# Kernel tuning notes

Hardware: AMD Instinct MI355X
Metric: run time of the kernel (lower is better)

Reference implementation:

```python
import jax, jax.numpy as jnp
import numpy as np

# Module config (from init_kwargs)
B, S = 2, 2048            # batch, prompt length
NH, D = 16, 64            # num query heads, head_size
NKV = 4                   # num kv heads
QPK = NH // NKV           # queries per kv head (GQA)
BLOCK = 128               # paged KV-cache block size
NBLOCKS = 64              # total cache blocks
SCALE = 0.125             # 1/sqrt(D)
NEG = -1e9                # causal mask value (finite for grad safety)


def setup_inputs() -> dict:
    key = jax.random.key(0)
    k1, k2, k3 = jax.random.split(key, 3)
    query = jax.random.normal(k1, (B, S, NH * D), jnp.float32)
    key_t = jax.random.normal(k2, (B, S, NKV * D), jnp.float32)
    value = jax.random.normal(k3, (B, S, NKV * D), jnp.float32)
    # kv_cache = [2, num_blocks, block_size, num_kv_heads, head_size]
    kv_cache = jnp.zeros((2, NBLOCKS, BLOCK, NKV, D), jnp.float32)
    # causal attn_bias [B, 1, 1, S, S] as set by the vLLM model runner
    i = jnp.arange(S)
    causal = jnp.where(i[None, :] <= i[:, None], 0.0, NEG).astype(jnp.float32)
    attn_bias = jnp.broadcast_to(causal[None, None, None], (B, 1, 1, S, S))
    # standard alibi slopes for 16 heads: 2^(-0.5*(h+1))
    alibi_slopes = 2.0 ** (-0.5 * (jnp.arange(NH, dtype=jnp.float32) + 1.0))
    # prompt writes B*S/BLOCK = 32 full blocks into the cache
    block_indices = jnp.arange(B * S // BLOCK, dtype=jnp.int32)
    return {"query": query, "key": key_t, "value": value, "kv_cache": kv_cache,
            "attn_bias": attn_bias, "alibi_slopes": alibi_slopes,
            "block_indices": block_indices}


def reference(query, key, value, kv_cache, attn_bias, alibi_slopes, block_indices):
    Bq, Sq, _ = query.shape
    q = query.reshape(Bq, Sq, NKV, QPK, D)   # [b, i, h, g, d]
    k = key.reshape(Bq, Sq, NKV, D)          # [b, j, h, d]
    v = value.reshape(Bq, Sq, NKV, D)

    # --- paged KV-cache scatter (VLLMKVCache.insert_or_update_cache, prompt path) ---
    k_blocks = key.reshape(-1, BLOCK, NKV, D)   # [n_used_blocks, block, h, d]
    v_blocks = value.reshape(-1, BLOCK, NKV, D)
    key_cache = kv_cache[0].at[block_indices].set(k_blocks)
    value_cache = kv_cache[1].at[block_indices].set(v_blocks)

    # --- _make_alibi_bias: (j - i) * slope, unflattened to [1, Hkv, qpk, S, S] ---
    ar = jnp.arange(Sq)
    diff = (ar[None, :] - ar[:, None]).astype(query.dtype)        # [S, S]
    pos_bias = alibi_slopes[:, None, None] * diff                  # [NH, S, S]
    pos_bias = pos_bias.reshape(1, NKV, QPK, Sq, Sq)
    bias = attn_bias + pos_bias                                    # [B, Hkv, qpk, S, S]

    # --- prompt_attention: matmul_qk -> softmax -> matmul_av (GQA) ---
    scores = jnp.einsum('bihgd,bjhd->bhgij', q, k) * SCALE + bias
    attn = jax.nn.softmax(scores, axis=-1)
    out = jnp.einsum('bhgij,bjhd->bihgd', attn, v).reshape(Bq, Sq, NH * D)
    return out, key_cache, value_cache
```

## Files before the change

kernel.cpp:

```cpp
#include <hip/hip_runtime.h>
#include <hip/hip_bf16.h>
#include <math.h>

#define BB    2
#define SS    2048
#define NHh   16
#define DD    64
#define NKV   4
#define BLKV  128
#define SCALE 0.125f

#define KT    64

typedef __attribute__((ext_vector_type(8))) short short8;
typedef __attribute__((ext_vector_type(4))) float f32x4;
typedef __attribute__((ext_vector_type(4))) int   i32x4;

template<int N> struct IC { static constexpr int v = N; };

__device__ inline short bf16c(float x) {
  __hip_bfloat16 h = __float2bfloat16(x);
  return *reinterpret_cast<short*>(&h);
}

__device__ inline int pk_bf16(float a, float b) {
  int d;
  asm("v_cvt_pk_bf16_f32 %0, %1, %2" : "=v"(d) : "v"(a), "v"(b));
  return d;
}

#define GLL16(g, l) __builtin_amdgcn_global_load_lds( \
    (const __attribute__((address_space(1))) void*)(g), \
    (__attribute__((address_space(3))) void*)(l), 16, 0, 0)

__global__ __launch_bounds__(256) void aux_kernel(
    const float* __restrict__ k, const float* __restrict__ v,
    const float* __restrict__ kvc, const int* __restrict__ bidx, int nidx,
    unsigned short* __restrict__ kimg, unsigned short* __restrict__ vimg,
    float* __restrict__ kc, float* __restrict__ vc)
{
  const int wg  = blockIdx.x;
  const int tid = threadIdx.x;
  if (wg < BB * NKV * (SS / KT)) {
    const int t   = wg & 31;
    const int hkv = (wg >> 5) & 3;
    const int b   = wg >> 7;
    const int j0  = t * KT;
    const float* kp = k + ((size_t)(b * SS + j0) * NKV + hkv) * DD;
    const float* vp = v + ((size_t)(b * SS + j0) * NKV + hkv) * DD;
    unsigned short* ki = kimg + (size_t)wg * 4096;
    unsigned short* vi = vimg + (size_t)wg * 4096;
    const int bi    = bidx[b * 16 + (t >> 1)];
    const int rowc0 = (t & 1) * 64;
    float* kcb = kc + (size_t)bi * (BLKV * NKV * DD);
    float* vcb = vc + (size_t)bi * (BLKV * NKV * DD);

    {
      const int jj = tid >> 2;
      const int sb = (tid & 3) * 2;
#pragma unroll
      for (int ss = 0; ss < 2; ++ss) {
        const int s  = sb + ss;
        const int d0 = (s ^ (jj & 7)) * 8;
        const float4 a = *(const float4*)(kp + jj * (NKV * DD) + d0);
        const float4 c = *(const float4*)(kp + jj * (NKV * DD) + d0 + 4);
        *(short8*)&ki[jj * 64 + s * 8] =
            (short8){bf16c(a.x), bf16c(a.y), bf16c(a.z), bf16c(a.w),
                     bf16c(c.x), bf16c(c.y), bf16c(c.z), bf16c(c.w)};
        float* kd = kcb + (rowc0 + jj) * (NKV * DD) + hkv * DD + d0;
        *(float4*)kd       = a;
        *(float4*)(kd + 4) = c;
      }
    }
    {
      const int d = tid & 63;
      const int w = tid >> 6;
#pragma unroll
      for (int ji = 0; ji < 2; ++ji) {
        const int jb = w * 2 + ji;
        float vv[8];
#pragma unroll
        for (int e = 0; e < 8; ++e)
          vv[e] = vp[(jb * 8 + e) * (NKV * DD) + d];
        const int s = jb ^ (d & 7);
        *(short8*)&vi[d * 64 + s * 8] =
            (short8){bf16c(vv[0]), bf16c(vv[1]), bf16c(vv[2]), bf16c(vv[3]),
                     bf16c(vv[4]), bf16c(vv[5]), bf16c(vv[6]), bf16c(vv[7])};
#pragma unroll
        for (int e = 0; e < 8; ++e)
          vcb[(rowc0 + jb * 8 + e) * (NKV * DD) + hkv * DD + d] = vv[e];
      }
    }
  } else {
    const int w2    = wg - BB * NKV * (SS / KT);
    const int blk   = w2 & 63;
    const int plane = w2 >> 6;
    int covered = 0;
    for (int m = 0; m < nidx; ++m) covered |= (bidx[m] == blk);
    if (covered) return;
    const float4* s4 = (const float4*)(kvc + (size_t)plane * (64 * BLKV * NKV * DD)
                                           + (size_t)blk * (BLKV * NKV * DD));
    float4* d4 = (float4*)((plane ? vc : kc) + (size_t)blk * (BLKV * NKV * DD));
#pragma unroll 4
    for (int i = tid; i < (BLKV * NKV * DD) / 4; i += 256) d4[i] = s4[i];
  }
}

__global__ __launch_bounds__(256) void attn_kernel(
    const float* __restrict__ q, const unsigned short* __restrict__ kimg,
    const unsigned short* __restrict__ vimg, const float* __restrict__ slopes,
    float* __restrict__ out)
{
  __shared__ __align__(16) unsigned short Kbuf[2][4096];
  __shared__ __align__(16) unsigned short Vbuf[2][4096];

  const int tid  = threadIdx.x;
  const int wave = tid >> 6;
  const int lane = tid & 63;
  const int cl   = lane & 15;
  const int g    = lane >> 4;

  const int grp   = blockIdx.x & 7;
  const int b     = grp >> 2;
  const int hkv   = grp & 3;
  const int local = blockIdx.x >> 3;
  const int h     = hkv * 4 + (local & 3);
  const int qt    = 31 - (local >> 2);

  const float L2E    = 1.44269504088896340736f;
  const float slope2 = slopes[h] * L2E;
  const float SC2    = SCALE * L2E;
  const int q_blk = qt * 64;
  const int q0    = q_blk + wave * 16;
  const int iq    = q0 + cl;

  short8 qf[2];
  {
    const float* qp = q + ((size_t)(b * SS + iq) * NHh + h) * DD;
#pragma unroll
    for (int kq = 0; kq < 2; ++kq) {
      const int d0 = kq * 32 + g * 8;
      const float4 a = *(const float4*)(qp + d0);
      const float4 c = *(const float4*)(qp + d0 + 4);
      qf[kq] = (short8){bf16c(a.x), bf16c(a.y), bf16c(a.z), bf16c(a.w),
                        bf16c(c.x), bf16c(c.y), bf16c(c.z), bf16c(c.w)};
    }
  }

  const float slope16 = slope2 * 16.f;
  const float slope64 = slope2 * 64.f;
  float ab = -slope2 * (float)iq;
  float cst[4];
#pragma unroll
  for (int r = 0; r < 4; ++r) cst[r] = slope2 * (float)(4 * g + r);

  const int src0 = cl + ((g & 1) << 5);
  const int src1 = src0 + 16;
  const bool gEven = (g < 2);

  float m_ = -INFINITY, l_ = 0.f;
  f32x4 acc[4];
#pragma unroll
  for (int dt = 0; dt < 4; ++dt) acc[dt] = (f32x4){0.f, 0.f, 0.f, 0.f};

  const char* kt0 = (const char*)kimg + (size_t)((b * NKV + hkv) * 32) * 8192;
  const char* vt0 = (const char*)vimg + (size_t)((b * NKV + hkv) * 32) * 8192;
  const int goff0 = wave * 2048 + lane * 16;
  const int ldst0 = wave * 2048;

  auto stage = [&](auto BUFC, int t) {
    constexpr int B = decltype(BUFC)::v;
    const char* kt = kt0 + (size_t)t * 8192 + goff0;
    const char* vt = vt0 + (size_t)t * 8192 + goff0;
    GLL16(kt,        (char*)&Kbuf[B][0] + ldst0);
    GLL16(kt + 1024, (char*)&Kbuf[B][0] + ldst0 + 1024);
    GLL16(vt,        (char*)&Vbuf[B][0] + ldst0);
    GLL16(vt + 1024, (char*)&Vbuf[B][0] + ldst0 + 1024);
  };

  auto tile = [&](auto BUFC, auto MSKC, int t) {
    constexpr int B    = decltype(BUFC)::v;
    constexpr bool MSK = decltype(MSKC)::v;
    const unsigned short* Kb = Kbuf[B];
    const unsigned short* Vb = Vbuf[B];

    f32x4 sc[4];
    __builtin_amdgcn_s_setprio(1);
#pragma unroll
    for (int jt = 0; jt < 4; ++jt) {
      const int rb = (jt * 16 + cl) * 64;
      const short8 kfA = *(const short8*)&Kb[rb + ((g       ^ (cl & 7)) << 3)];
      const short8 kfB = *(const short8*)&Kb[rb + (((4 | g) ^ (cl & 7)) << 3)];
      f32x4 s = (f32x4){0.f, 0.f, 0.f, 0.f};
      s = __builtin_amdgcn_mfma_f32_16x16x32_bf16(kfA, qf[0], s, 0, 0, 0);
      s = __builtin_amdgcn_mfma_f32_16x16x32_bf16(kfB, qf[1], s, 0, 0, 0);
      sc[jt] = s;
    }
    __builtin_amdgcn_s_setprio(0);

    float pm = -INFINITY;
#pragma unroll
    for (int jt = 0; jt < 4; ++jt) {
      const float ajt = ab + slope16 * (float)jt;
#pragma unroll
      for (int r = 0; r < 4; ++r) {
        float val = fmaf(sc[jt][r], SC2, ajt + cst[r]);
        if (MSK) {
          const int j = t * 64 + jt * 16 + 4 * g + r;
          val = (j <= iq) ? val : -INFINITY;
        }
        sc[jt][r] = val;
        pm = fmaxf(pm, val);
      }
    }
    pm = fmaxf(pm, __shfl_xor(pm, 16));
    pm = fmaxf(pm, __shfl_xor(pm, 32));

    if (!__all(pm - m_ <= 11.5f)) {
      const float mn = fmaxf(m_, pm);
      const float sf = exp2f(m_ - mn);
      m_ = mn;
      l_ *= sf;
#pragma unroll
      for (int dt = 0; dt < 4; ++dt)
#pragma unroll
        for (int r = 0; r < 4; ++r) acc[dt][r] *= sf;
    }

    float rs = 0.f;
#pragma unroll
    for (int jt = 0; jt < 4; ++jt) {
#pragma unroll
      for (int r = 0; r < 4; ++r) {
        const float p = exp2f(sc[jt][r] - m_);
        sc[jt][r] = p;
        rs += p;
      }
    }
    rs += __shfl_xor(rs, 16);
    rs += __shfl_xor(rs, 32);
    l_ += rs;

    __builtin_amdgcn_s_setprio(1);
#pragma unroll
    for (int ks = 0; ks < 2; ++ks) {
      const int E0 = pk_bf16(sc[2 * ks][0],     sc[2 * ks][1]);
      const int E1 = pk_bf16(sc[2 * ks][2],     sc[2 * ks][3]);
      const int O0 = pk_bf16(sc[2 * ks + 1][0], sc[2 * ks + 1][1]);
      const int O1 = pk_bf16(sc[2 * ks + 1][2], sc[2 * ks + 1][3]);
      const int d0e = __shfl(E0, src0), d0o = __shfl(O0, src0);
      const int d1e = __shfl(E1, src0), d1o = __shfl(O1, src0);
      const int d2e = __shfl(E0, src1), d2o = __shfl(O0, src1);
      const int d3e = __shfl(E1, src1), d3o = __shfl(O1, src1);
      i32x4 pd;
      pd[0] = gEven ? d0e : d0o;
      pd[1] = gEven ? d1e : d1o;
      pd[2] = gEven ? d2e : d2o;
      pd[3] = gEven ? d3e : d3o;
      const short8 pb = *(const short8*)&pd;
#pragma unroll
      for (int dt = 0; dt < 4; ++dt) {
        const short8 va = *(const short8*)
            &Vb[(dt * 16 + cl) * 64 + ((((ks << 2) | g) ^ (cl & 7)) << 3)];
        acc[dt] = __builtin_amdgcn_mfma_f32_16x16x32_bf16(va, pb, acc[dt], 0, 0, 0);
      }
    }
    __builtin_amdgcn_s_setprio(0);

    ab += slope64;
  };

  stage(IC<0>{}, 0);
  __syncthreads();

  const int nt = qt + 1;
  const int NU = nt - 1;
  int t = 0;
  while (t + 2 <= NU) {
    stage(IC<1>{}, t + 1);
    tile(IC<0>{}, IC<0>{}, t);
    __syncthreads();
    stage(IC<0>{}, t + 2);
    tile(IC<1>{}, IC<0>{}, t + 1);
    __syncthreads();
    t += 2;
  }
  if (t < NU) {
    stage(IC<1>{}, t + 1);
    tile(IC<0>{}, IC<0>{}, t);
    __syncthreads();
    tile(IC<1>{}, IC<1>{}, t + 1);
  } else {
    tile(IC<0>{}, IC<1>{}, t);
  }

  const float inv = 1.f / l_;
  float* op = out + ((size_t)(b * SS + iq) * NHh + h) * DD + 4 * g;
#pragma unroll
  for (int dt = 0; dt < 4; ++dt) {
    float4 o4;
    o4.x = acc[dt][0] * inv;
    o4.y = acc[dt][1] * inv;
    o4.z = acc[dt][2] * inv;
    o4.w = acc[dt][3] * inv;
    *(float4*)(op + dt * 16) = o4;
  }
}

extern "C" void kernel_launch(void* const* d_in, const int* in_sizes, int n_in,
                              void* d_out, int out_size, void* d_ws, size_t ws_size,
                              hipStream_t stream) {
  const float* q      = (const float*)d_in[0];
  const float* k      = (const float*)d_in[1];
  const float* v      = (const float*)d_in[2];
  const float* kvc    = (const float*)d_in[3];
  const float* slopes = (const float*)d_in[5];
  const int*   bidx   = (const int*)d_in[6];

  float* out = (float*)d_out;
  float* kc  = out + BB * SS * NHh * DD;
  float* vc  = kc + 64 * BLKV * NKV * DD;

  unsigned short* kimg = (unsigned short*)d_ws;
  unsigned short* vimg = kimg + (size_t)BB * NKV * 32 * 4096;

  const int nidx = in_sizes[6];

  aux_kernel<<<dim3(256 + 128), dim3(256), 0, stream>>>(
      k, v, kvc, bidx, nidx, kimg, vimg, kc, vc);

  attn_kernel<<<dim3(1024), dim3(256), 0, stream>>>(q, kimg, vimg, slopes, out);
}
```

Before: 65.62 us.

## Software-pipeline QK and PV across tiles with triple-buffered LDS

Restructures the attention main loop so the QK matmul of tile t is issued alongside the PV matmul of tile t-1, with the softmax of tile t following. The accumulator rescale is deferred until just before the next PV. LDS goes from double to triple buffering so the prefetch of tile t+1 can proceed during this overlap. The aim is to hide softmax/exp latency behind MFMA work. In exchange it uses more LDS and registers, and buffers are now chosen through runtime pointers instead of compile-time template constants, which may reduce occupancy or hurt code generation.

New measurement: 70.72 us. +7.8%, slower.

```diff
diff --git a/kernel.cpp b/kernel.cpp
--- a/kernel.cpp
+++ b/kernel.cpp
@@ -15,8 +15,6 @@
 typedef __attribute__((ext_vector_type(8))) short short8;
 typedef __attribute__((ext_vector_type(4))) float f32x4;
 typedef __attribute__((ext_vector_type(4))) int   i32x4;
-
-template<int N> struct IC { static constexpr int v = N; };
 
 __device__ inline short bf16c(float x) {
   __hip_bfloat16 h = __float2bfloat16(x);
@@ -111,8 +109,8 @@
     const unsigned short* __restrict__ vimg, const float* __restrict__ slopes,
     float* __restrict__ out)
 {
-  __shared__ __align__(16) unsigned short Kbuf[2][4096];
-  __shared__ __align__(16) unsigned short Vbuf[2][4096];
+  __shared__ __align__(16) unsigned short KB[3][4096];
+  __shared__ __align__(16) unsigned short VB[3][4096];
 
   const int tid  = threadIdx.x;
   const int wave = tid >> 6;
@@ -159,32 +157,29 @@
   const bool gEven = (g < 2);
 
   float m_ = -INFINITY, l_ = 0.f;
+  float sfp = 1.f;
+  bool  pend = false;
   f32x4 acc[4];
 #pragma unroll
   for (int dt = 0; dt < 4; ++dt) acc[dt] = (f32x4){0.f, 0.f, 0.f, 0.f};
+  short8 pb0, pb1;
+  f32x4 sc[4];
 
   const char* kt0 = (const char*)kimg + (size_t)((b * NKV + hkv) * 32) * 8192;
   const char* vt0 = (const char*)vimg + (size_t)((b * NKV + hkv) * 32) * 8192;
   const int goff0 = wave * 2048 + lane * 16;
   const int ldst0 = wave * 2048;
 
-  auto stage = [&](auto BUFC, int t) {
-    constexpr int B = decltype(BUFC)::v;
+  auto stage = [&](unsigned short* kb, unsigned short* vb, int t) {
     const char* kt = kt0 + (size_t)t * 8192 + goff0;
     const char* vt = vt0 + (size_t)t * 8192 + goff0;
-    GLL16(kt,        (char*)&Kbuf[B][0] + ldst0);
-    GLL16(kt + 1024, (char*)&Kbuf[B][0] + ldst0 + 1024);
-    GLL16(vt,        (char*)&Vbuf[B][0] + ldst0);
-    GLL16(vt + 1024, (char*)&Vbuf[B][0] + ldst0 + 1024);
-  };
-
-  auto tile = [&](auto BUFC, auto MSKC, int t) {
-    constexpr int B    = decltype(BUFC)::v;
-    constexpr bool MSK = decltype(MSKC)::v;
-    const unsigned short* Kb = Kbuf[B];
-    const unsigned short* Vb = Vbuf[B];
-
-    f32x4 sc[4];
+    GLL16(kt,        (char*)kb + ldst0);
+    GLL16(kt + 1024, (char*)kb + ldst0 + 1024);
+    GLL16(vt,        (char*)vb + ldst0);
+    GLL16(vt + 1024, (char*)vb + ldst0 + 1024);
+  };
+
+  auto qk = [&](const unsigned short* Kb) {
     __builtin_amdgcn_s_setprio(1);
 #pragma unroll
     for (int jt = 0; jt < 4; ++jt) {
@@ -197,34 +192,59 @@
       sc[jt] = s;
     }
     __builtin_amdgcn_s_setprio(0);
-
-    float pm = -INFINITY;
+  };
+
+  auto rescale = [&]() {
+    if (pend) {
+#pragma unroll
+      for (int dt = 0; dt < 4; ++dt)
+#pragma unroll
+        for (int r = 0; r < 4; ++r) acc[dt][r] *= sfp;
+      pend = false;
+    }
+  };
+
+  auto pv = [&](const unsigned short* Vb) {
+    __builtin_amdgcn_s_setprio(1);
+#pragma unroll
+    for (int ks = 0; ks < 2; ++ks) {
+      const short8 pbk = ks ? pb1 : pb0;
+#pragma unroll
+      for (int dt = 0; dt < 4; ++dt) {
+        const short8 va = *(const short8*)
+            &Vb[(dt * 16 + cl) * 64 + ((((ks << 2) | g) ^ (cl & 7)) << 3)];
+        acc[dt] = __builtin_amdgcn_mfma_f32_16x16x32_bf16(va, pbk, acc[dt], 0, 0, 0);
+      }
+    }
+    __builtin_amdgcn_s_setprio(0);
+  };
+
+  auto softmax = [&](int t, bool msk) {
+    float mj[4];
 #pragma unroll
     for (int jt = 0; jt < 4; ++jt) {
       const float ajt = ab + slope16 * (float)jt;
 #pragma unroll
       for (int r = 0; r < 4; ++r) {
         float val = fmaf(sc[jt][r], SC2, ajt + cst[r]);
-        if (MSK) {
+        if (msk) {
           const int j = t * 64 + jt * 16 + 4 * g + r;
           val = (j <= iq) ? val : -INFINITY;
         }
         sc[jt][r] = val;
-        pm = fmaxf(pm, val);
-      }
-    }
+      }
+      mj[jt] = fmaxf(fmaxf(sc[jt][0], sc[jt][1]), fmaxf(sc[jt][2], sc[jt][3]));
+    }
+    float pm = fmaxf(fmaxf(mj[0], mj[1]), fmaxf(mj[2], mj[3]));
     pm = fmaxf(pm, __shfl_xor(pm, 16));
     pm = fmaxf(pm, __shfl_xor(pm, 32));
 
     if (!__all(pm - m_ <= 11.5f)) {
       const float mn = fmaxf(m_, pm);
-      const float sf = exp2f(m_ - mn);
+      sfp = exp2f(m_ - mn);
       m_ = mn;
-      l_ *= sf;
-#pragma unroll
-      for (int dt = 0; dt < 4; ++dt)
-#pragma unroll
-        for (int r = 0; r < 4; ++r) acc[dt][r] *= sf;
+      l_ *= sfp;
+      pend = true;
     }
 
     float rs = 0.f;
@@ -241,7 +261,6 @@
     rs += __shfl_xor(rs, 32);
     l_ += rs;
 
-    __builtin_amdgcn_s_setprio(1);
 #pragma unroll
     for (int ks = 0; ks < 2; ++ks) {
       const int E0 = pk_bf16(sc[2 * ks][0],     sc[2 * ks][1]);
@@ -257,42 +276,36 @@
       pd[1] = gEven ? d1e : d1o;
       pd[2] = gEven ? d2e : d2o;
       pd[3] = gEven ? d3e : d3o;
-      const short8 pb = *(const short8*)&pd;
-#pragma unroll
-      for (int dt = 0; dt < 4; ++dt) {
-        const short8 va = *(const short8*)
-            &Vb[(dt * 16 + cl) * 64 + ((((ks << 2) | g) ^ (cl & 7)) << 3)];
-        acc[dt] = __builtin_amdgcn_mfma_f32_16x16x32_bf16(va, pb, acc[dt], 0, 0, 0);
-      }
-    }
-    __builtin_amdgcn_s_setprio(0);
-
+      if (ks == 0) pb0 = *(const short8*)&pd;
+      else         pb1 = *(const short8*)&pd;
+    }
     ab += slope64;
   };
 
-  stage(IC<0>{}, 0);
+  const int NU = qt;
+  stage(&KB[0][0], &VB[0][0], 0);
+  if (NU >= 1) stage(&KB[1][0], &VB[1][0], 1);
   __syncthreads();
 
-  const int nt = qt + 1;
-  const int NU = nt - 1;
-  int t = 0;
-  while (t + 2 <= NU) {
-    stage(IC<1>{}, t + 1);
-    tile(IC<0>{}, IC<0>{}, t);
+  qk(&KB[0][0]);
+  softmax(0, NU == 0);
+
+  unsigned short *kcur = &KB[1][0], *kprv = &KB[0][0], *knxt = &KB[2][0];
+  unsigned short *vcur = &VB[1][0], *vprv = &VB[0][0], *vnxt = &VB[2][0];
+
+  for (int t = 1; t <= NU; ++t) {
+    qk(kcur);
+    if (t < NU) stage(knxt, vnxt, t + 1);
+    rescale();
+    pv(vprv);
+    softmax(t, t == NU);
     __syncthreads();
-    stage(IC<0>{}, t + 2);
-    tile(IC<1>{}, IC<0>{}, t + 1);
-    __syncthreads();
-    t += 2;
+    unsigned short* tk = kprv; kprv = kcur; kcur = knxt; knxt = tk;
+    unsigned short* tv = vprv; vprv = vcur; vcur = vnxt; vnxt = tv;
   }
-  if (t < NU) {
-    stage(IC<1>{}, t + 1);
-    tile(IC<0>{}, IC<0>{}, t);
-    __syncthreads();
-    tile(IC<1>{}, IC<1>{}, t + 1);
-  } else {
-    tile(IC<0>{}, IC<1>{}, t);
-  }
+
+  rescale();
+  pv(vprv);
 
   const float inv = 1.f / l_;
   float* op = out + ((size_t)(b * SS + iq) * NHh + h) * DD + 4 * g;
```

## Pair short and long causal query tiles per workgroup with split-KV merge

Applied to the files above, without the earlier changes.

Each 512-thread workgroup now handles two query tiles, a short one (p) and a long one (31-p), so causal work is balanced across workgroups. Both wave groups share the K/V stream up to the short tile. After that, the second tile's KV range is split by column halves between the two groups, and the partial softmax results are merged through shared memory. This removes the tail imbalance of the triangular workload. The cost is larger workgroups, an extra LDS merge phase and half-width MFMA work per group in the second phase.

After: 64.10 us. 2.3% less time.

```diff
diff --git a/kernel.cpp b/kernel.cpp
--- a/kernel.cpp
+++ b/kernel.cpp
@@ -106,36 +106,41 @@
   }
 }
 
-__global__ __launch_bounds__(256) void attn_kernel(
+__global__ __launch_bounds__(512) void attn_kernel(
     const float* __restrict__ q, const unsigned short* __restrict__ kimg,
     const unsigned short* __restrict__ vimg, const float* __restrict__ slopes,
     float* __restrict__ out)
 {
-  __shared__ __align__(16) unsigned short Kbuf[2][4096];
-  __shared__ __align__(16) unsigned short Vbuf[2][4096];
+  __shared__ __align__(16) char smem[2 * 16384];
 
   const int tid  = threadIdx.x;
   const int wave = tid >> 6;
   const int lane = tid & 63;
   const int cl   = lane & 15;
   const int g    = lane >> 4;
+  const int group = wave >> 2;
+  const int wi    = wave & 3;
 
   const int grp   = blockIdx.x & 7;
   const int b     = grp >> 2;
   const int hkv   = grp & 3;
   const int local = blockIdx.x >> 3;
   const int h     = hkv * 4 + (local & 3);
-  const int qt    = 31 - (local >> 2);
+  const int p     = local >> 2;
+  const int qtA   = p;
+  const int qtB   = 31 - p;
 
   const float L2E    = 1.44269504088896340736f;
   const float slope2 = slopes[h] * L2E;
   const float SC2    = SCALE * L2E;
-  const int q_blk = qt * 64;
-  const int q0    = q_blk + wave * 16;
-  const int iq    = q0 + cl;
+  const float slope16 = slope2 * 16.f;
+  const float slope64 = slope2 * 64.f;
+
+  int myqt = group ? qtB : qtA;
+  int iq   = myqt * 64 + wi * 16 + cl;
 
   short8 qf[2];
-  {
+  auto loadQ = [&]() {
     const float* qp = q + ((size_t)(b * SS + iq) * NHh + h) * DD;
 #pragma unroll
     for (int kq = 0; kq < 2; ++kq) {
@@ -145,10 +150,9 @@
       qf[kq] = (short8){bf16c(a.x), bf16c(a.y), bf16c(a.z), bf16c(a.w),
                         bf16c(c.x), bf16c(c.y), bf16c(c.z), bf16c(c.w)};
     }
-  }
-
-  const float slope16 = slope2 * 16.f;
-  const float slope64 = slope2 * 64.f;
+  };
+  loadQ();
+
   float ab = -slope2 * (float)iq;
   float cst[4];
 #pragma unroll
@@ -165,29 +169,25 @@
 
   const char* kt0 = (const char*)kimg + (size_t)((b * NKV + hkv) * 32) * 8192;
   const char* vt0 = (const char*)vimg + (size_t)((b * NKV + hkv) * 32) * 8192;
-  const int goff0 = wave * 2048 + lane * 16;
-  const int ldst0 = wave * 2048;
-
-  auto stage = [&](auto BUFC, int t) {
-    constexpr int B = decltype(BUFC)::v;
-    const char* kt = kt0 + (size_t)t * 8192 + goff0;
-    const char* vt = vt0 + (size_t)t * 8192 + goff0;
-    GLL16(kt,        (char*)&Kbuf[B][0] + ldst0);
-    GLL16(kt + 1024, (char*)&Kbuf[B][0] + ldst0 + 1024);
-    GLL16(vt,        (char*)&Vbuf[B][0] + ldst0);
-    GLL16(vt + 1024, (char*)&Vbuf[B][0] + ldst0 + 1024);
+
+  auto stage = [&](int buf, int t) {
+    char* base = smem + buf * 16384 + wave * 1024;
+    const char* src = kt0 + (size_t)t * 8192 + wave * 1024 + lane * 16;
+    const char* srv = vt0 + (size_t)t * 8192 + wave * 1024 + lane * 16;
+    GLL16(src, base);
+    GLL16(srv, base + 8192);
   };
 
-  auto tile = [&](auto BUFC, auto MSKC, int t) {
-    constexpr int B    = decltype(BUFC)::v;
-    constexpr bool MSK = decltype(MSKC)::v;
-    const unsigned short* Kb = Kbuf[B];
-    const unsigned short* Vb = Vbuf[B];
+  auto tcore = [&](auto JTBC, auto JTEC, int buf, int t, bool msk) {
+    constexpr int JTB = decltype(JTBC)::v;
+    constexpr int JTE = decltype(JTEC)::v;
+    const unsigned short* Kb = (const unsigned short*)(smem + buf * 16384);
+    const unsigned short* Vb = (const unsigned short*)(smem + buf * 16384 + 8192);
 
     f32x4 sc[4];
     __builtin_amdgcn_s_setprio(1);
 #pragma unroll
-    for (int jt = 0; jt < 4; ++jt) {
+    for (int jt = JTB; jt < JTE; ++jt) {
       const int rb = (jt * 16 + cl) * 64;
       const short8 kfA = *(const short8*)&Kb[rb + ((g       ^ (cl & 7)) << 3)];
       const short8 kfB = *(const short8*)&Kb[rb + (((4 | g) ^ (cl & 7)) << 3)];
@@ -198,20 +198,29 @@
     }
     __builtin_amdgcn_s_setprio(0);
 
+#pragma unroll
+    for (int jt = JTB; jt < JTE; ++jt) {
+      const float ajt = ab + slope16 * (float)jt;
+#pragma unroll
+      for (int r = 0; r < 4; ++r)
+        sc[jt][r] = fmaf(sc[jt][r], SC2, ajt + cst[r]);
+    }
+    if (msk) {
+#pragma unroll
+      for (int jt = JTB; jt < JTE; ++jt)
+#pragma unroll
+        for (int r = 0; r < 4; ++r) {
+          const int j = t * 64 + jt * 16 + 4 * g + r;
+          if (j > iq) sc[jt][r] = -INFINITY;
+        }
+    }
+
     float pm = -INFINITY;
 #pragma unroll
-    for (int jt = 0; jt < 4; ++jt) {
-      const float ajt = ab + slope16 * (float)jt;
-#pragma unroll
-      for (int r = 0; r < 4; ++r) {
-        float val = fmaf(sc[jt][r], SC2, ajt + cst[r]);
-        if (MSK) {
-          const int j = t * 64 + jt * 16 + 4 * g + r;
-          val = (j <= iq) ? val : -INFINITY;
-        }
-        sc[jt][r] = val;
-        pm = fmaxf(pm, val);
-      }
+    for (int jt = JTB; jt < JTE; ++jt) {
+      const float a01 = fmaxf(sc[jt][0], sc[jt][1]);
+      const float a23 = fmaxf(sc[jt][2], sc[jt][3]);
+      pm = fmaxf(pm, fmaxf(a01, a23));
     }
     pm = fmaxf(pm, __shfl_xor(pm, 16));
     pm = fmaxf(pm, __shfl_xor(pm, 32));
@@ -229,21 +238,20 @@
 
     float rs = 0.f;
 #pragma unroll
-    for (int jt = 0; jt < 4; ++jt) {
+    for (int jt = JTB; jt < JTE; ++jt)
 #pragma unroll
       for (int r = 0; r < 4; ++r) {
-        const float p = exp2f(sc[jt][r] - m_);
-        sc[jt][r] = p;
-        rs += p;
+        const float pp = exp2f(sc[jt][r] - m_);
+        sc[jt][r] = pp;
+        rs += pp;
       }
-    }
     rs += __shfl_xor(rs, 16);
     rs += __shfl_xor(rs, 32);
     l_ += rs;
 
     __builtin_amdgcn_s_setprio(1);
 #pragma unroll
-    for (int ks = 0; ks < 2; ++ks) {
+    for (int ks = JTB / 2; ks < JTE / 2; ++ks) {
       const int E0 = pk_bf16(sc[2 * ks][0],     sc[2 * ks][1]);
       const int E1 = pk_bf16(sc[2 * ks][2],     sc[2 * ks][3]);
       const int O0 = pk_bf16(sc[2 * ks + 1][0], sc[2 * ks + 1][1]);
@@ -270,40 +278,80 @@
     ab += slope64;
   };
 
-  stage(IC<0>{}, 0);
+  int buf = 0;
+  stage(0, 0);
   __syncthreads();
-
-  const int nt = qt + 1;
-  const int NU = nt - 1;
-  int t = 0;
-  while (t + 2 <= NU) {
-    stage(IC<1>{}, t + 1);
-    tile(IC<0>{}, IC<0>{}, t);
+  for (int t = 0; t <= qtA; ++t) {
+    stage(buf ^ 1, t + 1);
+    tcore(IC<0>{}, IC<4>{}, buf, t, (group == 0) && (t == qtA));
     __syncthreads();
-    stage(IC<0>{}, t + 2);
-    tile(IC<1>{}, IC<0>{}, t + 1);
+    buf ^= 1;
+  }
+
+  if (group == 0) {
+    const float inv = 1.f / l_;
+    float* op = out + ((size_t)(b * SS + iq) * NHh + h) * DD + 4 * g;
+#pragma unroll
+    for (int dt = 0; dt < 4; ++dt) {
+      float4 o4;
+      o4.x = acc[dt][0] * inv;
+      o4.y = acc[dt][1] * inv;
+      o4.z = acc[dt][2] * inv;
+      o4.w = acc[dt][3] * inv;
+      *(float4*)(op + dt * 16) = o4;
+    }
+    iq = qtB * 64 + wi * 16 + cl;
+    loadQ();
+    m_ = -INFINITY; l_ = 0.f;
+#pragma unroll
+    for (int dt = 0; dt < 4; ++dt) acc[dt] = (f32x4){0.f, 0.f, 0.f, 0.f};
+    ab = slope2 * (float)(64 * (qtA + 1) - iq);
+  }
+
+  for (int t = qtA + 1; t <= qtB; ++t) {
+    if (t < qtB) stage(buf ^ 1, t + 1);
+    const bool msk = (t == qtB);
+    if (group) tcore(IC<2>{}, IC<4>{}, buf, t, msk);
+    else       tcore(IC<0>{}, IC<2>{}, buf, t, msk);
     __syncthreads();
-    t += 2;
-  }
-  if (t < NU) {
-    stage(IC<1>{}, t + 1);
-    tile(IC<0>{}, IC<0>{}, t);
-    __syncthreads();
-    tile(IC<1>{}, IC<1>{}, t + 1);
-  } else {
-    tile(IC<0>{}, IC<1>{}, t);
-  }
-
-  const float inv = 1.f / l_;
-  float* op = out + ((size_t)(b * SS + iq) * NHh + h) * DD + 4 * g;
-#pragma unroll
-  for (int dt = 0; dt < 4; ++dt) {
-    float4 o4;
-    o4.x = acc[dt][0] * inv;
-    o4.y = acc[dt][1] * inv;
-    o4.z = acc[dt][2] * inv;
-    o4.w = acc[dt][3] * inv;
-    *(float4*)(op + dt * 16) = o4;
+    buf ^= 1;
+  }
+
+  float* accA = (float*)smem;
+  float* mlA  = (float*)(smem + 4 * 16 * 72 * 4);
+  if (group == 0) {
+    float* ar = accA + (wi * 16 + cl) * 72 + 4 * g;
+#pragma unroll
+    for (int dt = 0; dt < 4; ++dt) {
+      float4 a4;
+      a4.x = acc[dt][0]; a4.y = acc[dt][1]; a4.z = acc[dt][2]; a4.w = acc[dt][3];
+      *(float4*)(ar + dt * 16) = a4;
+    }
+    if (g == 0) {
+      mlA[(wi * 2 + 0) * 16 + cl] = m_;
+      mlA[(wi * 2 + 1) * 16 + cl] = l_;
+    }
+  }
+  __syncthreads();
+  if (group == 1) {
+    const float mA = mlA[(wi * 2 + 0) * 16 + cl];
+    const float lA = mlA[(wi * 2 + 1) * 16 + cl];
+    const float M  = fmaxf(m_, mA);
+    const float eB = exp2f(m_ - M);
+    const float eA = exp2f(mA - M);
+    const float inv = 1.f / (l_ * eB + lA * eA);
+    const float* ar = accA + (wi * 16 + cl) * 72 + 4 * g;
+    float* op = out + ((size_t)(b * SS + iq) * NHh + h) * DD + 4 * g;
+#pragma unroll
+    for (int dt = 0; dt < 4; ++dt) {
+      const float4 a4 = *(const float4*)(ar + dt * 16);
+      float4 o4;
+      o4.x = (acc[dt][0] * eB + a4.x * eA) * inv;
+      o4.y = (acc[dt][1] * eB + a4.y * eA) * inv;
+      o4.z = (acc[dt][2] * eB + a4.z * eA) * inv;
+      o4.w = (acc[dt][3] * eB + a4.w * eA) * inv;
+      *(float4*)(op + dt * 16) = o4;
+    }
   }
 }
 
@@ -329,5 +377,5 @@
   aux_kernel<<<dim3(256 + 128), dim3(256), 0, stream>>>(
       k, v, kvc, bidx, nidx, kimg, vimg, kc, vc);
 
-  attn_kernel<<<dim3(1024), dim3(256), 0, stream>>>(q, kimg, vimg, slopes, out);
-}
+  attn_kernel<<<dim3(512), dim3(512), 0, stream>>>(q, kimg, vimg, slopes, out);
+}
```

## Switch attention to 32x32x16 MFMA with split-KV waves and merged softmax

Applied to the files above, without the earlier changes.

Replaces the 16x16x32 MFMA tiling with 32x32x16 MFMAs. Each pair of waves now shares 32 query rows and splits each 64-key tile into two 32-key halves, and the two partial softmax states are merged through LDS at the end. The aux kernel writes K and V into a single interleaved, MFMA-fragment-ordered image per tile, so LDS reads become plain lane-contiguous loads with no swizzle. The aim is fewer MFMA issues and cross-lane shuffles, at the cost of an extra LDS reduction and barrier, and one wave idling on the diagonal tile.

New measurement: 72.43 us. 1.1x slower.

```diff
diff --git a/kernel.cpp b/kernel.cpp
--- a/kernel.cpp
+++ b/kernel.cpp
@@ -10,11 +10,9 @@
 #define BLKV  128
 #define SCALE 0.125f
 
-#define KT    64
-
-typedef __attribute__((ext_vector_type(8))) short short8;
-typedef __attribute__((ext_vector_type(4))) float f32x4;
-typedef __attribute__((ext_vector_type(4))) int   i32x4;
+typedef __attribute__((ext_vector_type(8)))  short short8;
+typedef __attribute__((ext_vector_type(16))) float f32x16;
+typedef __attribute__((ext_vector_type(4)))  int   i32x4;
 
 template<int N> struct IC { static constexpr int v = N; };
 
@@ -36,45 +34,44 @@
 __global__ __launch_bounds__(256) void aux_kernel(
     const float* __restrict__ k, const float* __restrict__ v,
     const float* __restrict__ kvc, const int* __restrict__ bidx, int nidx,
-    unsigned short* __restrict__ kimg, unsigned short* __restrict__ vimg,
-    float* __restrict__ kc, float* __restrict__ vc)
+    char* __restrict__ img, float* __restrict__ kc, float* __restrict__ vc)
 {
   const int wg  = blockIdx.x;
   const int tid = threadIdx.x;
-  if (wg < BB * NKV * (SS / KT)) {
+  if (wg < BB * NKV * 32) {
     const int t   = wg & 31;
     const int hkv = (wg >> 5) & 3;
     const int b   = wg >> 7;
-    const int j0  = t * KT;
-    const float* kp = k + ((size_t)(b * SS + j0) * NKV + hkv) * DD;
-    const float* vp = v + ((size_t)(b * SS + j0) * NKV + hkv) * DD;
-    unsigned short* ki = kimg + (size_t)wg * 4096;
-    unsigned short* vi = vimg + (size_t)wg * 4096;
+    const float* kp = k + ((size_t)(b * SS + t * 64) * NKV + hkv) * DD;
+    const float* vp = v + ((size_t)(b * SS + t * 64) * NKV + hkv) * DD;
+    char* ti = img + (size_t)wg * 16384;
     const int bi    = bidx[b * 16 + (t >> 1)];
     const int rowc0 = (t & 1) * 64;
     float* kcb = kc + (size_t)bi * (BLKV * NKV * DD);
     float* vcb = vc + (size_t)bi * (BLKV * NKV * DD);
 
     {
-      const int jj = tid >> 2;
-      const int sb = (tid & 3) * 2;
-#pragma unroll
-      for (int ss = 0; ss < 2; ++ss) {
-        const int s  = sb + ss;
-        const int d0 = (s ^ (jj & 7)) * 8;
-        const float4 a = *(const float4*)(kp + jj * (NKV * DD) + d0);
-        const float4 c = *(const float4*)(kp + jj * (NKV * DD) + d0 + 4);
-        *(short8*)&ki[jj * 64 + s * 8] =
+      const int jg  = tid & 63;
+      const int cs2 = tid >> 6;
+#pragma unroll
+      for (int ch = 0; ch < 2; ++ch) {
+        const int c  = cs2 * 2 + ch;
+        const int d0 = c * 8;
+        const float4 a  = *(const float4*)(kp + jg * (NKV * DD) + d0);
+        const float4 cc = *(const float4*)(kp + jg * (NKV * DD) + d0 + 4);
+        *(short8*)(ti + (jg >> 5) * 4096 + (cs2 * 64 + ch * 32 + (jg & 31)) * 16) =
             (short8){bf16c(a.x), bf16c(a.y), bf16c(a.z), bf16c(a.w),
-                     bf16c(c.x), bf16c(c.y), bf16c(c.z), bf16c(c.w)};
-        float* kd = kcb + (rowc0 + jj) * (NKV * DD) + hkv * DD + d0;
+                     bf16c(cc.x), bf16c(cc.y), bf16c(cc.z), bf16c(cc.w)};
+        float* kd = kcb + (rowc0 + jg) * (NKV * DD) + hkv * DD + d0;
         *(float4*)kd       = a;
-        *(float4*)(kd + 4) = c;
+        *(float4*)(kd + 4) = cc;
       }
     }
     {
-      const int d = tid & 63;
-      const int w = tid >> 6;
+      const int d   = tid & 63;
+      const int w   = tid >> 6;
+      const int dt  = d >> 5;
+      const int d32 = d & 31;
 #pragma unroll
       for (int ji = 0; ji < 2; ++ji) {
         const int jb = w * 2 + ji;
@@ -82,8 +79,9 @@
 #pragma unroll
         for (int e = 0; e < 8; ++e)
           vv[e] = vp[(jb * 8 + e) * (NKV * DD) + d];
-        const int s = jb ^ (d & 7);
-        *(short8*)&vi[d * 64 + s * 8] =
+        const int half = jb >> 2, qq = jb & 3, ks = qq >> 1, h2 = qq & 1;
+        *(short8*)(ti + 8192 + half * 4096 +
+                   ((dt * 2 + ks) * 64 + h2 * 32 + d32) * 16) =
             (short8){bf16c(vv[0]), bf16c(vv[1]), bf16c(vv[2]), bf16c(vv[3]),
                      bf16c(vv[4]), bf16c(vv[5]), bf16c(vv[6]), bf16c(vv[7])};
 #pragma unroll
@@ -92,7 +90,7 @@
       }
     }
   } else {
-    const int w2    = wg - BB * NKV * (SS / KT);
+    const int w2    = wg - BB * NKV * 32;
     const int blk   = w2 & 63;
     const int plane = w2 >> 6;
     int covered = 0;
@@ -107,113 +105,101 @@
 }
 
 __global__ __launch_bounds__(256) void attn_kernel(
-    const float* __restrict__ q, const unsigned short* __restrict__ kimg,
-    const unsigned short* __restrict__ vimg, const float* __restrict__ slopes,
-    float* __restrict__ out)
+    const float* __restrict__ q, const char* __restrict__ img,
+    const float* __restrict__ slopes, float* __restrict__ out)
 {
-  __shared__ __align__(16) unsigned short Kbuf[2][4096];
-  __shared__ __align__(16) unsigned short Vbuf[2][4096];
+  __shared__ __align__(16) char smem[2 * 16384];
 
   const int tid  = threadIdx.x;
   const int wave = tid >> 6;
   const int lane = tid & 63;
-  const int cl   = lane & 15;
-  const int g    = lane >> 4;
+  const int ql   = lane & 31;
+  const int h2   = lane >> 5;
+  const int half = wave & 1;
+  const int qsel = wave >> 1;
 
   const int grp   = blockIdx.x & 7;
   const int b     = grp >> 2;
   const int hkv   = grp & 3;
   const int local = blockIdx.x >> 3;
-  const int h     = hkv * 4 + (local & 3);
+  const int hh    = hkv * 4 + (local & 3);
   const int qt    = 31 - (local >> 2);
 
   const float L2E    = 1.44269504088896340736f;
-  const float slope2 = slopes[h] * L2E;
+  const float slope2 = slopes[hh] * L2E;
   const float SC2    = SCALE * L2E;
-  const int q_blk = qt * 64;
-  const int q0    = q_blk + wave * 16;
-  const int iq    = q0 + cl;
-
-  short8 qf[2];
+  const int qbase = qt * 64 + qsel * 32;
+  const int qrow  = qbase + ql;
+
+  short8 qf[4];
   {
-    const float* qp = q + ((size_t)(b * SS + iq) * NHh + h) * DD;
-#pragma unroll
-    for (int kq = 0; kq < 2; ++kq) {
-      const int d0 = kq * 32 + g * 8;
+    const float* qp = q + ((size_t)(b * SS + qrow) * NHh + hh) * DD;
+#pragma unroll
+    for (int ks = 0; ks < 4; ++ks) {
+      const int d0 = ks * 16 + h2 * 8;
       const float4 a = *(const float4*)(qp + d0);
       const float4 c = *(const float4*)(qp + d0 + 4);
-      qf[kq] = (short8){bf16c(a.x), bf16c(a.y), bf16c(a.z), bf16c(a.w),
+      qf[ks] = (short8){bf16c(a.x), bf16c(a.y), bf16c(a.z), bf16c(a.w),
                         bf16c(c.x), bf16c(c.y), bf16c(c.z), bf16c(c.w)};
     }
   }
 
-  const float slope16 = slope2 * 16.f;
-  const float slope64 = slope2 * 64.f;
-  float ab = -slope2 * (float)iq;
-  float cst[4];
-#pragma unroll
-  for (int r = 0; r < 4; ++r) cst[r] = slope2 * (float)(4 * g + r);
-
-  const int src0 = cl + ((g & 1) << 5);
-  const int src1 = src0 + 16;
-  const bool gEven = (g < 2);
+  const int jqoff = half * 32 + 4 * h2 - qrow;
+  float sl_lo[4], sl_hi[4];
+#pragma unroll
+  for (int i = 0; i < 4; ++i) { sl_lo[i] = slope2 * i; sl_hi[i] = slope2 * (8 * i); }
 
   float m_ = -INFINITY, l_ = 0.f;
-  f32x4 acc[4];
-#pragma unroll
-  for (int dt = 0; dt < 4; ++dt) acc[dt] = (f32x4){0.f, 0.f, 0.f, 0.f};
-
-  const char* kt0 = (const char*)kimg + (size_t)((b * NKV + hkv) * 32) * 8192;
-  const char* vt0 = (const char*)vimg + (size_t)((b * NKV + hkv) * 32) * 8192;
-  const int goff0 = wave * 2048 + lane * 16;
-  const int ldst0 = wave * 2048;
+  f32x16 acc0, acc1;
+#pragma unroll
+  for (int r = 0; r < 16; ++r) { acc0[r] = 0.f; acc1[r] = 0.f; }
+
+  const char* tile0 = img + (size_t)((b * NKV + hkv) * 32) * 16384;
 
   auto stage = [&](auto BUFC, int t) {
     constexpr int B = decltype(BUFC)::v;
-    const char* kt = kt0 + (size_t)t * 8192 + goff0;
-    const char* vt = vt0 + (size_t)t * 8192 + goff0;
-    GLL16(kt,        (char*)&Kbuf[B][0] + ldst0);
-    GLL16(kt + 1024, (char*)&Kbuf[B][0] + ldst0 + 1024);
-    GLL16(vt,        (char*)&Vbuf[B][0] + ldst0);
-    GLL16(vt + 1024, (char*)&Vbuf[B][0] + ldst0 + 1024);
+    const char* src = tile0 + (size_t)t * 16384 + wave * 4096 + lane * 16;
+    char* dst = smem + B * 16384 + wave * 4096;
+#pragma unroll
+    for (int i = 0; i < 4; ++i) GLL16(src + i * 1024, dst + i * 1024);
   };
 
-  auto tile = [&](auto BUFC, auto MSKC, int t) {
-    constexpr int B    = decltype(BUFC)::v;
+  auto tcore = [&](auto BUFC, auto MSKC, int t) {
+    constexpr int  B   = decltype(BUFC)::v;
     constexpr bool MSK = decltype(MSKC)::v;
-    const unsigned short* Kb = Kbuf[B];
-    const unsigned short* Vb = Vbuf[B];
-
-    f32x4 sc[4];
+    const char* base = smem + B * 16384;
+    const char* Kb = base + half * 4096;
+    const char* Vb = base + 8192 + half * 4096;
+
+    f32x16 S;
+#pragma unroll
+    for (int r = 0; r < 16; ++r) S[r] = 0.f;
     __builtin_amdgcn_s_setprio(1);
 #pragma unroll
-    for (int jt = 0; jt < 4; ++jt) {
-      const int rb = (jt * 16 + cl) * 64;
-      const short8 kfA = *(const short8*)&Kb[rb + ((g       ^ (cl & 7)) << 3)];
-      const short8 kfB = *(const short8*)&Kb[rb + (((4 | g) ^ (cl & 7)) << 3)];
-      f32x4 s = (f32x4){0.f, 0.f, 0.f, 0.f};
-      s = __builtin_amdgcn_mfma_f32_16x16x32_bf16(kfA, qf[0], s, 0, 0, 0);
-      s = __builtin_amdgcn_mfma_f32_16x16x32_bf16(kfB, qf[1], s, 0, 0, 0);
-      sc[jt] = s;
+    for (int ks = 0; ks < 4; ++ks) {
+      const short8 kf = *(const short8*)(Kb + ks * 1024 + lane * 16);
+      S = __builtin_amdgcn_mfma_f32_32x32x16_bf16(kf, qf[ks], S, 0, 0, 0);
     }
     __builtin_amdgcn_s_setprio(0);
 
-    float pm = -INFINITY;
-#pragma unroll
-    for (int jt = 0; jt < 4; ++jt) {
-      const float ajt = ab + slope16 * (float)jt;
-#pragma unroll
-      for (int r = 0; r < 4; ++r) {
-        float val = fmaf(sc[jt][r], SC2, ajt + cst[r]);
-        if (MSK) {
-          const int j = t * 64 + jt * 16 + 4 * g + r;
-          val = (j <= iq) ? val : -INFINITY;
-        }
-        sc[jt][r] = val;
-        pm = fmaxf(pm, val);
-      }
-    }
-    pm = fmaxf(pm, __shfl_xor(pm, 16));
+    const int   dbase = t * 64 + jqoff;
+    const float abh   = slope2 * (float)dbase;
+#pragma unroll
+    for (int r = 0; r < 16; ++r) {
+      float val = fmaf(S[r], SC2, abh + sl_hi[r >> 2] + sl_lo[r & 3]);
+      if (MSK) {
+        const int jp = (r & 3) + 8 * (r >> 2);
+        if (dbase + jp > 0) val = -INFINITY;
+      }
+      S[r] = val;
+    }
+
+    float t0 = fmaxf(S[0], S[1]),  t1 = fmaxf(S[2], S[3]);
+    float t2 = fmaxf(S[4], S[5]),  t3 = fmaxf(S[6], S[7]);
+    float t4 = fmaxf(S[8], S[9]),  t5 = fmaxf(S[10], S[11]);
+    float t6 = fmaxf(S[12], S[13]), t7 = fmaxf(S[14], S[15]);
+    t0 = fmaxf(t0, t1); t2 = fmaxf(t2, t3); t4 = fmaxf(t4, t5); t6 = fmaxf(t6, t7);
+    float pm = fmaxf(fmaxf(t0, t2), fmaxf(t4, t6));
     pm = fmaxf(pm, __shfl_xor(pm, 32));
 
     if (!__all(pm - m_ <= 11.5f)) {
@@ -222,88 +208,115 @@
       m_ = mn;
       l_ *= sf;
 #pragma unroll
-      for (int dt = 0; dt < 4; ++dt)
-#pragma unroll
-        for (int r = 0; r < 4; ++r) acc[dt][r] *= sf;
+      for (int r = 0; r < 16; ++r) { acc0[r] *= sf; acc1[r] *= sf; }
     }
 
     float rs = 0.f;
 #pragma unroll
-    for (int jt = 0; jt < 4; ++jt) {
-#pragma unroll
-      for (int r = 0; r < 4; ++r) {
-        const float p = exp2f(sc[jt][r] - m_);
-        sc[jt][r] = p;
-        rs += p;
-      }
-    }
-    rs += __shfl_xor(rs, 16);
+    for (int r = 0; r < 16; ++r) {
+      const float p = exp2f(S[r] - m_);
+      S[r] = p;
+      rs += p;
+    }
     rs += __shfl_xor(rs, 32);
     l_ += rs;
 
+    const int P0 = pk_bf16(S[0],  S[1]),  P1 = pk_bf16(S[2],  S[3]);
+    const int P2 = pk_bf16(S[4],  S[5]),  P3 = pk_bf16(S[6],  S[7]);
+    const int P4 = pk_bf16(S[8],  S[9]),  P5 = pk_bf16(S[10], S[11]);
+    const int P6 = pk_bf16(S[12], S[13]), P7 = pk_bf16(S[14], S[15]);
+    const int sxP0 = __shfl_xor(P0, 32), sxP1 = __shfl_xor(P1, 32);
+    const int sxP2 = __shfl_xor(P2, 32), sxP3 = __shfl_xor(P3, 32);
+    const int sxP4 = __shfl_xor(P4, 32), sxP5 = __shfl_xor(P5, 32);
+    const int sxP6 = __shfl_xor(P6, 32), sxP7 = __shfl_xor(P7, 32);
+    i32x4 pd0, pd1;
+    pd0[0] = h2 ? sxP2 : P0;
+    pd0[1] = h2 ? sxP3 : P1;
+    pd0[2] = h2 ? P2   : sxP0;
+    pd0[3] = h2 ? P3   : sxP1;
+    pd1[0] = h2 ? sxP6 : P4;
+    pd1[1] = h2 ? sxP7 : P5;
+    pd1[2] = h2 ? P6   : sxP4;
+    pd1[3] = h2 ? P7   : sxP5;
+    const short8 pf0 = *(const short8*)&pd0;
+    const short8 pf1 = *(const short8*)&pd1;
+
     __builtin_amdgcn_s_setprio(1);
-#pragma unroll
-    for (int ks = 0; ks < 2; ++ks) {
-      const int E0 = pk_bf16(sc[2 * ks][0],     sc[2 * ks][1]);
-      const int E1 = pk_bf16(sc[2 * ks][2],     sc[2 * ks][3]);
-      const int O0 = pk_bf16(sc[2 * ks + 1][0], sc[2 * ks + 1][1]);
-      const int O1 = pk_bf16(sc[2 * ks + 1][2], sc[2 * ks + 1][3]);
-      const int d0e = __shfl(E0, src0), d0o = __shfl(O0, src0);
-      const int d1e = __shfl(E1, src0), d1o = __shfl(O1, src0);
-      const int d2e = __shfl(E0, src1), d2o = __shfl(O0, src1);
-      const int d3e = __shfl(E1, src1), d3o = __shfl(O1, src1);
-      i32x4 pd;
-      pd[0] = gEven ? d0e : d0o;
-      pd[1] = gEven ? d1e : d1o;
-      pd[2] = gEven ? d2e : d2o;
-      pd[3] = gEven ? d3e : d3o;
-      const short8 pb = *(const short8*)&pd;
-#pragma unroll
-      for (int dt = 0; dt < 4; ++dt) {
-        const short8 va = *(const short8*)
-            &Vb[(dt * 16 + cl) * 64 + ((((ks << 2) | g) ^ (cl & 7)) << 3)];
-        acc[dt] = __builtin_amdgcn_mfma_f32_16x16x32_bf16(va, pb, acc[dt], 0, 0, 0);
-      }
+    {
+      const short8 va00 = *(const short8*)(Vb + 0 * 1024 + lane * 16);
+      const short8 va01 = *(const short8*)(Vb + 1 * 1024 + lane * 16);
+      const short8 va10 = *(const short8*)(Vb + 2 * 1024 + lane * 16);
+      const short8 va11 = *(const short8*)(Vb + 3 * 1024 + lane * 16);
+      acc0 = __builtin_amdgcn_mfma_f32_32x32x16_bf16(va00, pf0, acc0, 0, 0, 0);
+      acc0 = __builtin_amdgcn_mfma_f32_32x32x16_bf16(va01, pf1, acc0, 0, 0, 0);
+      acc1 = __builtin_amdgcn_mfma_f32_32x32x16_bf16(va10, pf0, acc1, 0, 0, 0);
+      acc1 = __builtin_amdgcn_mfma_f32_32x32x16_bf16(va11, pf1, acc1, 0, 0, 0);
     }
     __builtin_amdgcn_s_setprio(0);
-
-    ab += slope64;
   };
 
   stage(IC<0>{}, 0);
   __syncthreads();
-
-  const int nt = qt + 1;
-  const int NU = nt - 1;
   int t = 0;
-  while (t + 2 <= NU) {
+  while (t + 2 <= qt) {
     stage(IC<1>{}, t + 1);
-    tile(IC<0>{}, IC<0>{}, t);
+    tcore(IC<0>{}, IC<0>{}, t);
     __syncthreads();
     stage(IC<0>{}, t + 2);
-    tile(IC<1>{}, IC<0>{}, t + 1);
+    tcore(IC<1>{}, IC<0>{}, t + 1);
     __syncthreads();
     t += 2;
   }
-  if (t < NU) {
-    stage(IC<1>{}, t + 1);
-    tile(IC<0>{}, IC<0>{}, t);
+  if (t == qt) {
+    if (wave != 1) tcore(IC<0>{}, IC<1>{}, qt);
+  } else {
+    stage(IC<1>{}, qt);
+    tcore(IC<0>{}, IC<0>{}, t);
     __syncthreads();
-    tile(IC<1>{}, IC<1>{}, t + 1);
-  } else {
-    tile(IC<0>{}, IC<1>{}, t);
-  }
-
-  const float inv = 1.f / l_;
-  float* op = out + ((size_t)(b * SS + iq) * NHh + h) * DD + 4 * g;
-#pragma unroll
-  for (int dt = 0; dt < 4; ++dt) {
-    float4 o4;
-    o4.x = acc[dt][0] * inv;
-    o4.y = acc[dt][1] * inv;
-    o4.z = acc[dt][2] * inv;
-    o4.w = acc[dt][3] * inv;
-    *(float4*)(op + dt * 16) = o4;
+    if (wave != 1) tcore(IC<1>{}, IC<1>{}, qt);
+  }
+  __syncthreads();
+
+  float* mb = (float*)(smem + qsel * 8704);
+  if (half == 1) {
+#pragma unroll
+    for (int dt = 0; dt < 2; ++dt)
+#pragma unroll
+      for (int pr = 0; pr < 8; ++pr) {
+        float2 x;
+        x.x = dt ? acc1[pr * 2] : acc0[pr * 2];
+        x.y = dt ? acc1[pr * 2 + 1] : acc0[pr * 2 + 1];
+        *(float2*)(mb + (dt * 8 + pr) * 128 + lane * 2) = x;
+      }
+    mb[2048 + lane] = m_;
+    mb[2112 + lane] = l_;
+  }
+  __syncthreads();
+  if (half == 0) {
+    const float m1 = mb[2048 + lane];
+    const float l1 = mb[2112 + lane];
+    const float M  = fmaxf(m_, m1);
+    const float e0 = exp2f(m_ - M);
+    const float e1 = exp2f(m1 - M);
+    const float linv = 1.f / (l_ * e0 + l1 * e1);
+    float* op = out + ((size_t)(b * SS + qrow) * NHh + hh) * DD;
+#pragma unroll
+    for (int dt = 0; dt < 2; ++dt)
+#pragma unroll
+      for (int rq = 0; rq < 4; ++rq) {
+        const float2 x0 = *(const float2*)(mb + (dt * 8 + rq * 2) * 128 + lane * 2);
+        const float2 x1 = *(const float2*)(mb + (dt * 8 + rq * 2 + 1) * 128 + lane * 2);
+        float4 o4;
+        const float a0 = dt ? acc1[rq * 4 + 0] : acc0[rq * 4 + 0];
+        const float a1 = dt ? acc1[rq * 4 + 1] : acc0[rq * 4 + 1];
+        const float a2 = dt ? acc1[rq * 4 + 2] : acc0[rq * 4 + 2];
+        const float a3 = dt ? acc1[rq * 4 + 3] : acc0[rq * 4 + 3];
+        o4.x = (a0 * e0 + x0.x * e1) * linv;
+        o4.y = (a1 * e0 + x0.y * e1) * linv;
+        o4.z = (a2 * e0 + x1.x * e1) * linv;
+        o4.w = (a3 * e0 + x1.y * e1) * linv;
+        *(float4*)(op + dt * 32 + rq * 8 + 4 * h2) = o4;
+      }
   }
 }
 
@@ -321,13 +334,11 @@
   float* kc  = out + BB * SS * NHh * DD;
   float* vc  = kc + 64 * BLKV * NKV * DD;
 
-  unsigned short* kimg = (unsigned short*)d_ws;
-  unsigned short* vimg = kimg + (size_t)BB * NKV * 32 * 4096;
-
+  char* img = (char*)d_ws;
   const int nidx = in_sizes[6];
 
   aux_kernel<<<dim3(256 + 128), dim3(256), 0, stream>>>(
-      k, v, kvc, bidx, nidx, kimg, vimg, kc, vc);
-
-  attn_kernel<<<dim3(1024), dim3(256), 0, stream>>>(q, kimg, vimg, slopes, out);
-}
+      k, v, kvc, bidx, nidx, img, kc, vc);
+
+  attn_kernel<<<dim3(1024), dim3(256), 0, stream>>>(q, img, slopes, out);
+}
```
